# Kernel tuning notes

Measured on AMD Instinct MI355X. Metric: run time of the kernel, lower is better.

The kernel has to match this reference:

```python
import jax, jax.numpy as jnp
import numpy as np

H = 256; NH = 4; DH = H // NH
NT, NS, NV = 4096, 2048, 1024
E1, E2, E3 = 65536, 16384, 32768
LN_EPS = 1e-5


def setup_inputs() -> dict:
    key = jax.random.key(0)
    ks = jax.random.split(key, 40)
    def nrm(i, shape):
        return jax.random.normal(ks[i], shape, jnp.float32) * 0.05
    inp = {
        "x_term": jax.random.normal(ks[0], (NT, H), jnp.float32),
        "x_symbol": jax.random.normal(ks[1], (NS, H), jnp.float32),
        "x_var": jax.random.normal(ks[2], (NV, H), jnp.float32),
        "ha_src": jax.random.randint(ks[3], (E1,), 0, NT),
        "ha_dst": jax.random.randint(ks[4], (E1,), 0, NT),
        "so_src": jax.random.randint(ks[5], (E2,), 0, NT),
        "so_dst": jax.random.randint(ks[6], (E2,), 0, NS),
        "vo_src": jax.random.randint(ks[7], (E3,), 0, NV),
        "vo_dst": jax.random.randint(ks[8], (E3,), 0, NT),
        # SAGEConv params for the 4 term-destination relations
        "Wl_rha": nrm(9, (H, H)),  "bl_rha": nrm(10, (H,)), "Wr_rha": nrm(11, (H, H)),
        "Wl_ha":  nrm(12, (H, H)), "bl_ha":  nrm(13, (H,)), "Wr_ha":  nrm(14, (H, H)),
        "Wl_rsym": nrm(15, (H, H)), "bl_rsym": nrm(16, (H,)), "Wr_rsym": nrm(17, (H, H)),
        "Wl_var": nrm(18, (H, H)), "bl_var": nrm(19, (H,)), "Wr_var": nrm(20, (H, H)),
        "ln_g": jnp.ones((H,), jnp.float32),
        "ln_b": jnp.zeros((H,), jnp.float32),
        "in_proj_w": nrm(21, (3 * H, H)),
        "in_proj_b": nrm(22, (3 * H,)),
        "out_proj_w": nrm(23, (H, H)),
        "out_proj_b": nrm(24, (H,)),
        "post_w": nrm(25, (H, H)),
        "post_b": nrm(26, (H,)),
    }
    return inp


def _sage(x_src, x_dst, src, dst, Wl, bl, Wr, num_dst):
    # PyG SAGEConv: lin_l(mean_j x_src[j]) + lin_r(x_dst)
    msg = x_src[src]                                            # [E, H] gather
    s = jax.ops.segment_sum(msg, dst, num_segments=num_dst)     # [N_dst, H] scatter-add
    cnt = jax.ops.segment_sum(jnp.ones((src.shape[0],), x_src.dtype), dst,
                              num_segments=num_dst)
    agg = s / jnp.maximum(cnt, 1.0)[:, None]
    return agg @ Wl.T + bl + x_dst @ Wr.T


def _layernorm(x, g, b):
    mu = jnp.mean(x, axis=-1, keepdims=True)
    var = jnp.mean(jnp.square(x - mu), axis=-1, keepdims=True)
    return (x - mu) * jax.lax.rsqrt(var + LN_EPS) * g + b


def _mha(x, in_w, in_b, out_w, out_b):
    # torch MultiheadAttention (eval, batch=1, self-attention)
    qkv = x @ in_w.T + in_b                       # [N, 3H]
    q, k, v = jnp.split(qkv, 3, axis=-1)
    def heads(t):
        return t.reshape(-1, NH, DH).transpose(1, 0, 2)  # [NH, N, DH]
    q, k, v = heads(q), heads(k), heads(v)
    scores = jnp.einsum("hqd,hkd->hqk", q, k) / np.sqrt(DH).astype(np.float32)
    a = jax.nn.softmax(scores, axis=-1)
    o = jnp.einsum("hqk,hkd->hqd", a, v)          # [NH, N, DH]
    o = o.transpose(1, 0, 2).reshape(-1, H)
    return o @ out_w.T + out_b


def reference(x_term, x_symbol, x_var,
              ha_src, ha_dst, so_src, so_dst, vo_src, vo_dst,
              Wl_rha, bl_rha, Wr_rha, Wl_ha, bl_ha, Wr_ha,
              Wl_rsym, bl_rsym, Wr_rsym, Wl_var, bl_var, Wr_var,
              ln_g, ln_b, in_proj_w, in_proj_b, out_proj_w, out_proj_b,
              post_w, post_b):
    nt = x_term.shape[0]
    # HeteroConv(aggr='sum') over the 4 relations whose destination is 'term'
    conv_term = (
        _sage(x_term, x_term, ha_dst, ha_src, Wl_rha, bl_rha, Wr_rha, nt)    # rev_has_arg
        + _sage(x_term, x_term, ha_src, ha_dst, Wl_ha, bl_ha, Wr_ha, nt)     # has_arg
        + _sage(x_symbol, x_term, so_dst, so_src, Wl_rsym, bl_rsym, Wr_rsym, nt)  # rev_symbol_of
        + _sage(x_var, x_term, vo_src, vo_dst, Wl_var, bl_var, Wr_var, nt)   # var_occurrence
    )
    term_out = _layernorm(conv_term + x_term, ln_g, ln_b)  # dropout is identity in eval
    attn_out = _mha(term_out, in_proj_w, in_proj_b, out_proj_w, out_proj_b)
    post = jax.nn.relu(attn_out @ post_w.T + post_b)
    term_final = post + term_out
    return term_final
```

## Files before the change

kernel.cpp:

```cpp
#include <hip/hip_runtime.h>
#include <hip/hip_bf16.h>

#define H 256
#define NT 4096
#define NHEAD 4
#define E1 65536
#define E2 16384
#define E3 32768
#define TOTE (2 * E1 + E2 + E3)
#define LN_EPS 1e-5f
#define SPLIT 4

typedef __hip_bfloat16 bf16;
typedef short bf16x8 __attribute__((ext_vector_type(8)));
typedef float f32x4 __attribute__((ext_vector_type(4)));

__device__ __forceinline__ float b2f(bf16 v) { return __bfloat162float(v); }
__device__ __forceinline__ float u2f(unsigned short u) {
    unsigned int x = ((unsigned int)u) << 16;
    return __uint_as_float(x);
}
__device__ __forceinline__ unsigned short f2u(float f) {
    bf16 h = __float2bfloat16(f);
    unsigned short v;
    __builtin_memcpy(&v, &h, 2);
    return v;
}
__device__ __forceinline__ float ldin(const void* p, size_t i, bool isbf) {
    return isbf ? b2f(((const bf16*)p)[i]) : ((const float*)p)[i];
}
__device__ __forceinline__ void gload_lds16(const void* g, void* l) {
    __builtin_amdgcn_global_load_lds(
        (const __attribute__((address_space(1))) unsigned int*)g,
        (__attribute__((address_space(3))) unsigned int*)l, 16, 0, 0);
}

__global__ __launch_bounds__(256) void k_count4(const int* __restrict__ s0, const int* __restrict__ s1,
                                                const int* __restrict__ s2, const int* __restrict__ s3,
                                                int* __restrict__ cnt) {
    int i = blockIdx.x * 256 + threadIdx.x;
    int r, e;
    if (i < E1) { r = 0; e = i; }
    else if (i < 2 * E1) { r = 1; e = i - E1; }
    else if (i < 2 * E1 + E2) { r = 2; e = i - 2 * E1; }
    else if (i < TOTE) { r = 3; e = i - 2 * E1 - E2; }
    else return;
    const int* s = (r == 0) ? s0 : (r == 1) ? s1 : (r == 2) ? s2 : s3;
    atomicAdd(&cnt[r * NT + s[e]], 1);
}

__global__ __launch_bounds__(256) void k_scan(const int* __restrict__ cnt, int* __restrict__ offs,
                                              int* __restrict__ cursor,
                                              const unsigned int* __restrict__ lng,
                                              unsigned int* __restrict__ flag) {
    __shared__ int tot[256];
    int t = threadIdx.x, r = blockIdx.x;
    if (r == 0 && t == 0) *flag = (lng[0] == 0x3F803F80u) ? 1u : 0u;
    const int* c = cnt + r * NT;
    int* o = offs + r * (NT + 1);
    int* cur = cursor + r * NT;
    int base = t * 16;
    int local[16];
    int sum = 0;
#pragma unroll
    for (int j = 0; j < 16; j++) { local[j] = c[base + j]; sum += local[j]; }
    tot[t] = sum;
    __syncthreads();
    if (t == 0) {
        int run = 0;
        for (int i = 0; i < 256; i++) { int v = tot[i]; tot[i] = run; run += v; }
        o[NT] = run;
    }
    __syncthreads();
    int run = tot[t];
#pragma unroll
    for (int j = 0; j < 16; j++) { o[base + j] = run; cur[base + j] = run; run += local[j]; }
}

__global__ __launch_bounds__(256) void k_fill(const int* __restrict__ s0, const int* __restrict__ s1,
                                              const int* __restrict__ s2, const int* __restrict__ s3,
                                              const int* __restrict__ g0, const int* __restrict__ g1,
                                              const int* __restrict__ g2, const int* __restrict__ g3,
                                              int* __restrict__ cursor, int* __restrict__ csr) {
    int i = blockIdx.x * 256 + threadIdx.x;
    int r, e, rb;
    if (i < E1) { r = 0; e = i; rb = 0; }
    else if (i < 2 * E1) { r = 1; e = i - E1; rb = E1; }
    else if (i < 2 * E1 + E2) { r = 2; e = i - 2 * E1; rb = 2 * E1; }
    else if (i < TOTE) { r = 3; e = i - 2 * E1 - E2; rb = 2 * E1 + E2; }
    else return;
    const int* s = (r == 0) ? s0 : (r == 1) ? s1 : (r == 2) ? s2 : s3;
    const int* g = (r == 0) ? g0 : (r == 1) ? g1 : (r == 2) ? g2 : g3;
    int d = s[e];
    int pos = atomicAdd(&cursor[r * NT + d], 1);
    csr[rb + pos] = g[e];
}

__global__ __launch_bounds__(256) void k_gprep(
    const void* __restrict__ x0, const void* __restrict__ x1,
    const void* __restrict__ x2, const void* __restrict__ x3,
    const int* __restrict__ offs, const int* __restrict__ csr,
    bf16* __restrict__ aggs,
    const void* __restrict__ Wl0, const void* __restrict__ Wl1,
    const void* __restrict__ Wl2, const void* __restrict__ Wl3,
    const void* __restrict__ Wr0, const void* __restrict__ Wr1,
    const void* __restrict__ Wr2, const void* __restrict__ Wr3,
    const void* __restrict__ bb0, const void* __restrict__ bb1,
    const void* __restrict__ bb2, const void* __restrict__ bb3,
    bf16* __restrict__ Bcat, float* __restrict__ bsum,
    const unsigned int* __restrict__ flag) {
    const int bid = blockIdx.x, tid = threadIdx.x;
    const bool isbf = (*flag != 0u);
    if (bid < 4096) {
        int y = bid >> 10;
        int i = (bid & 1023) * 4 + (tid >> 6);
        int lane = tid & 63;
        const void* x = (y == 0) ? x0 : (y == 1) ? x1 : (y == 2) ? x2 : x3;
        static const int rbase[4] = {0, E1, 2 * E1, 2 * E1 + E2};
        const int* o = offs + y * (NT + 1);
        const int* cs = csr + rbase[y];
        int b = o[i], e = o[i + 1];
        float ax = 0.f, ay = 0.f, az = 0.f, aw = 0.f;
        float bx = 0.f, by = 0.f, bz = 0.f, bw = 0.f;
        int j = b;
        if (isbf) {
            for (; j + 2 <= e; j += 2) {
                int s0 = cs[j], s1 = cs[j + 1];
                ushort4 u0 = *(const ushort4*)((const unsigned short*)x + (size_t)s0 * H + lane * 4);
                ushort4 u1 = *(const ushort4*)((const unsigned short*)x + (size_t)s1 * H + lane * 4);
                ax += u2f(u0.x); ay += u2f(u0.y); az += u2f(u0.z); aw += u2f(u0.w);
                bx += u2f(u1.x); by += u2f(u1.y); bz += u2f(u1.z); bw += u2f(u1.w);
            }
            if (j < e) {
                int s = cs[j];
                ushort4 u = *(const ushort4*)((const unsigned short*)x + (size_t)s * H + lane * 4);
                ax += u2f(u.x); ay += u2f(u.y); az += u2f(u.z); aw += u2f(u.w);
            }
        } else {
            for (; j + 2 <= e; j += 2) {
                int s0 = cs[j], s1 = cs[j + 1];
                float4 v0 = *(const float4*)((const float*)x + (size_t)s0 * H + lane * 4);
                float4 v1 = *(const float4*)((const float*)x + (size_t)s1 * H + lane * 4);
                ax += v0.x; ay += v0.y; az += v0.z; aw += v0.w;
                bx += v1.x; by += v1.y; bz += v1.z; bw += v1.w;
            }
            if (j < e) {
                int s = cs[j];
                float4 v = *(const float4*)((const float*)x + (size_t)s * H + lane * 4);
                ax += v.x; ay += v.y; az += v.z; aw += v.w;
            }
        }
        ax += bx; ay += by; az += bz; aw += bw;
        float inv = 1.0f / fmaxf((float)(e - b), 1.0f);
        *(ushort4*)((unsigned short*)aggs + ((size_t)y * NT + i) * H + lane * 4) =
            make_ushort4(f2u(ax * inv), f2u(ay * inv), f2u(az * inv), f2u(aw * inv));
    } else {
        int idx = (bid - 4096) * 256 + tid;
        int n = idx / 1280, k = idx % 1280;
        float v;
        if (k < 1024) {
            const void* W = (k < 256) ? Wl0 : (k < 512) ? Wl1 : (k < 768) ? Wl2 : Wl3;
            v = ldin(W, (size_t)n * 256 + (k & 255), isbf);
        } else {
            size_t o = (size_t)n * 256 + (k - 1024);
            v = ldin(Wr0, o, isbf) + ldin(Wr1, o, isbf) + ldin(Wr2, o, isbf) + ldin(Wr3, o, isbf);
        }
        ((unsigned short*)Bcat)[idx] = f2u(v);
        if (idx < 256)
            bsum[idx] = ldin(bb0, idx, isbf) + ldin(bb1, idx, isbf) +
                        ldin(bb2, idx, isbf) + ldin(bb3, idx, isbf);
    }
}

__global__ __launch_bounds__(256) void k_convln(
    const bf16* __restrict__ aggs, const bf16* __restrict__ Bcat, const float* __restrict__ bsum,
    const void* __restrict__ xt, const void* __restrict__ gw, const void* __restrict__ gb,
    bf16* __restrict__ term, const unsigned int* __restrict__ flag) {
    __shared__ unsigned short Asm[160 * 16 * 8];
    __shared__ unsigned short Bsm[2][8 * 256 * 8];
    __shared__ float redS[4][16];
    const bool isbf = (*flag != 0u);
    const int tid = threadIdx.x;
    const int w = tid >> 6, lane = tid & 63;
    const int col = lane & 15, quad = lane >> 4;
    const int m0 = blockIdx.x * 16;

#pragma unroll
    for (int t = 0; t < 8; t++) {
        int c2 = t * 256 + tid;
        int row = c2 & 15, kq = c2 >> 4;
        gload_lds16((const unsigned short*)aggs + ((size_t)(kq >> 5) * NT + m0 + row) * 256 + (kq & 31) * 8,
                    &Asm[(t * 256 + w * 64) * 8]);
    }
    if (isbf) {
#pragma unroll
        for (int t = 8; t < 10; t++) {
            int c2 = t * 256 + tid;
            int row = c2 & 15, kq = c2 >> 4;
            gload_lds16((const unsigned short*)xt + (size_t)(m0 + row) * 256 + (kq - 128) * 8,
                        &Asm[(t * 256 + w * 64) * 8]);
        }
    } else {
#pragma unroll
        for (int t = 8; t < 10; t++) {
            int c2 = t * 256 + tid;
            int row = c2 & 15, kq = c2 >> 4;
            const float* xf = (const float*)xt;
            bf16x8 a;
#pragma unroll
            for (int j = 0; j < 8; j++)
                a[j] = (short)f2u(xf[(size_t)(m0 + row) * 256 + (kq - 128) * 8 + j]);
            *(bf16x8*)&Asm[c2 * 8] = a;
        }
    }
    asm volatile("s_waitcnt vmcnt(0) lgkmcnt(0)" ::: "memory");
    __builtin_amdgcn_s_barrier();

    auto stageB = [&](int k0, int buf) {
#pragma unroll
        for (int t = 0; t < 8; t++) {
            gload_lds16((const unsigned short*)Bcat + (size_t)tid * 1280 + k0 + t * 8,
                        &Bsm[buf][(t * 256 + w * 64) * 8]);
        }
    };
    f32x4 acc[4];
#pragma unroll
    for (int dt = 0; dt < 4; dt++) acc[dt] = (f32x4){0.f, 0.f, 0.f, 0.f};

    stageB(0, 0);
    stageB(64, 1);
    for (int k0 = 0; k0 < 1280; k0 += 64) {
        const int cur = (k0 >> 6) & 1;
        if (k0 + 64 < 1280) {
            asm volatile("s_waitcnt vmcnt(8)" ::: "memory");
        } else {
            asm volatile("s_waitcnt vmcnt(0)" ::: "memory");
        }
        __builtin_amdgcn_s_barrier();
        __builtin_amdgcn_sched_barrier(0);
#pragma unroll
        for (int ch = 0; ch < 2; ch++) {
            bf16x8 a = *(const bf16x8*)&Asm[(((k0 >> 3) + ch * 4 + quad) * 16 + col) * 8];
#pragma unroll
            for (int dt = 0; dt < 4; dt++) {
                bf16x8 b = *(const bf16x8*)&Bsm[cur][((ch * 4 + quad) * 256 + w * 64 + dt * 16 + col) * 8];
                acc[dt] = __builtin_amdgcn_mfma_f32_16x16x32_bf16(a, b, acc[dt], 0, 0, 0);
            }
        }
        __builtin_amdgcn_sched_barrier(0);
        __builtin_amdgcn_s_barrier();
        if (k0 + 128 < 1280) stageB(k0 + 128, cur);
    }

#pragma unroll
    for (int dt = 0; dt < 4; dt++) {
        int n = w * 64 + dt * 16 + col;
        float bsv = bsum[n];
#pragma unroll
        for (int r = 0; r < 4; r++) {
            int m = m0 + quad * 4 + r;
            acc[dt][r] += bsv + ldin(xt, (size_t)m * 256 + n, isbf);
        }
    }
    float mu[4], rs_[4];
#pragma unroll
    for (int r = 0; r < 4; r++) {
        float s = acc[0][r] + acc[1][r] + acc[2][r] + acc[3][r];
#pragma unroll
        for (int mk = 1; mk <= 8; mk <<= 1) s += __shfl_xor(s, mk);
        if (col == 0) redS[w][quad * 4 + r] = s;
    }
    __syncthreads();
#pragma unroll
    for (int r = 0; r < 4; r++) {
        int m = quad * 4 + r;
        mu[r] = (redS[0][m] + redS[1][m] + redS[2][m] + redS[3][m]) * (1.0f / 256.0f);
    }
    __syncthreads();
#pragma unroll
    for (int r = 0; r < 4; r++) {
        float s2 = 0.f;
#pragma unroll
        for (int dt = 0; dt < 4; dt++) {
            float d = acc[dt][r] - mu[r];
            s2 += d * d;
        }
#pragma unroll
        for (int mk = 1; mk <= 8; mk <<= 1) s2 += __shfl_xor(s2, mk);
        if (col == 0) redS[w][quad * 4 + r] = s2;
    }
    __syncthreads();
#pragma unroll
    for (int r = 0; r < 4; r++) {
        int m = quad * 4 + r;
        float var = (redS[0][m] + redS[1][m] + redS[2][m] + redS[3][m]) * (1.0f / 256.0f);
        rs_[r] = rsqrtf(var + LN_EPS);
    }
#pragma unroll
    for (int dt = 0; dt < 4; dt++) {
        int n = w * 64 + dt * 16 + col;
        float gv = ldin(gw, n, isbf), bv = ldin(gb, n, isbf);
#pragma unroll
        for (int r = 0; r < 4; r++) {
            int m = m0 + quad * 4 + r;
            term[(size_t)m * 256 + n] = __float2bfloat16((acc[dt][r] - mu[r]) * rs_[r] * gv + bv);
        }
    }
}

template <int AMODE, int EPI>
__global__ __launch_bounds__(256) void k_gemm(
    const void* __restrict__ A, const void* __restrict__ A2, const float* __restrict__ ml,
    const void* __restrict__ B, const void* __restrict__ bias,
    const bf16* __restrict__ resid, bf16* __restrict__ vt, void* __restrict__ outp,
    int M, int N, int K, const unsigned int* __restrict__ flag) {
    __shared__ unsigned short Asm[32 * 64 * 8];
    __shared__ unsigned short Bsm[32 * 64 * 8];
    const bool isbf = (*flag != 0u);
    const int tid = threadIdx.x;
    const int w = tid >> 6, lane = tid & 63;
    const int col = lane & 15, quad = lane >> 4;
    const int m0 = blockIdx.x * 64, n0 = blockIdx.y * 64;
    const int srow = tid & 63, skq = tid >> 6;
    const int am = m0 + srow;

    if (AMODE == 0) {
#pragma unroll
        for (int c = 0; c < 8; c++) {
            gload_lds16((const unsigned short*)A + (size_t)(m0 + lane) * K + skq * 64 + c * 8,
                        &Asm[((skq * 8 + c) * 64) * 8]);
        }
    } else {
        float l0 = ml[(size_t)(0 * NHEAD + skq) * NT + am];
        float l1 = ml[(size_t)(1 * NHEAD + skq) * NT + am];
        float l2 = ml[(size_t)(2 * NHEAD + skq) * NT + am];
        float l3 = ml[(size_t)(3 * NHEAD + skq) * NT + am];
        float iw = 1.0f / (l0 + l1 + l2 + l3);
#pragma unroll
        for (int c = 0; c < 8; c++) {
            int k = skq * 64 + c * 8;
            bf16x8 o0 = *(const bf16x8*)((const unsigned short*)A + (size_t)am * H + k);
            bf16x8 o1 = *(const bf16x8*)((const unsigned short*)A + ((size_t)NT + am) * H + k);
            bf16x8 o2 = *(const bf16x8*)((const unsigned short*)A2 + (size_t)am * H + k);
            bf16x8 o3 = *(const bf16x8*)((const unsigned short*)A2 + ((size_t)NT + am) * H + k);
            bf16x8 areg;
#pragma unroll
            for (int j = 0; j < 8; j++)
                areg[j] = (short)f2u((l0 * u2f((unsigned short)o0[j]) + l1 * u2f((unsigned short)o1[j]) +
                                      l2 * u2f((unsigned short)o2[j]) + l3 * u2f((unsigned short)o3[j])) * iw);
            *(bf16x8*)&Asm[((skq * 8 + c) * 64 + srow) * 8] = areg;
        }
    }
    if (isbf) {
#pragma unroll
        for (int c = 0; c < 8; c++) {
            gload_lds16((const unsigned short*)B + (size_t)(n0 + lane) * K + skq * 64 + c * 8,
                        &Bsm[((skq * 8 + c) * 64) * 8]);
        }
    } else {
#pragma unroll
        for (int c = 0; c < 8; c++) {
            size_t bi = (size_t)(n0 + srow) * K + skq * 64 + c * 8;
            bf16x8 breg;
#pragma unroll
            for (int j = 0; j < 8; j++) breg[j] = (short)f2u(((const float*)B)[bi + j]);
            *(bf16x8*)&Bsm[((skq * 8 + c) * 64 + srow) * 8] = breg;
        }
    }
    __syncthreads();

    f32x4 acc[4];
#pragma unroll
    for (int dt = 0; dt < 4; dt++) acc[dt] = (f32x4){0.f, 0.f, 0.f, 0.f};
#pragma unroll
    for (int kk = 0; kk < 8; kk++) {
        bf16x8 a = *(const bf16x8*)&Asm[((kk * 4 + quad) * 64 + w * 16 + col) * 8];
#pragma unroll
        for (int dt = 0; dt < 4; dt++) {
            bf16x8 b = *(const bf16x8*)&Bsm[((kk * 4 + quad) * 64 + dt * 16 + col) * 8];
            acc[dt] = __builtin_amdgcn_mfma_f32_16x16x32_bf16(a, b, acc[dt], 0, 0, 0);
        }
    }
#pragma unroll
    for (int dt = 0; dt < 4; dt++) {
        int n = n0 + dt * 16 + col;
        float bv = ldin(bias, n, isbf);
        if (EPI == 3 && n0 >= 512) {
            int m = m0 + w * 16 + quad * 4;
            *(ushort4*)((unsigned short*)vt + (size_t)(n - 512) * NT + m) =
                make_ushort4(f2u(acc[dt][0] + bv), f2u(acc[dt][1] + bv),
                             f2u(acc[dt][2] + bv), f2u(acc[dt][3] + bv));
            continue;
        }
#pragma unroll
        for (int r = 0; r < 4; r++) {
            int m = m0 + w * 16 + quad * 4 + r;
            float v = acc[dt][r] + bv;
            if (EPI == 3) {
                ((bf16*)outp)[(size_t)m * 512 + n] = __float2bfloat16(v);
            } else if (EPI == 2) {
                size_t off = (size_t)m * N + n;
                v = fmaxf(v, 0.f);
                v += b2f(resid[off]);
                ((float*)outp)[off] = v;
            } else {
                ((bf16*)outp)[(size_t)m * N + n] = __float2bfloat16(v);
            }
        }
    }
    (void)M;
}

__global__ __launch_bounds__(256) void k_attn(const bf16* __restrict__ qkvQK,
                                              const bf16* __restrict__ vt,
                                              bf16* __restrict__ opart01,
                                              bf16* __restrict__ opart23,
                                              float* __restrict__ ml) {
    __shared__ unsigned short Ksm[2][8 * 64 * 8];
    __shared__ unsigned short Vsm[2][8 * 64 * 8];
    const int h = blockIdx.y, sp = blockIdx.z;
    const int q0 = blockIdx.x * 64;
    const int tid = threadIdx.x;
    const int w = tid >> 6, lane = tid & 63;
    const int col = lane & 15, quad = lane >> 4;
    const unsigned short* qk = (const unsigned short*)qkvQK;
    const unsigned short* vp = (const unsigned short*)vt;

    bf16x8 aQ[2];
#pragma unroll
    for (int ch = 0; ch < 2; ch++)
        aQ[ch] = *(const bf16x8*)(qk + (size_t)(q0 + w * 16 + col) * 512 +
                                  h * 64 + ch * 32 + quad * 8);

    f32x4 O[4];
#pragma unroll
    for (int dt = 0; dt < 4; dt++) O[dt] = (f32x4){0.f, 0.f, 0.f, 0.f};
    float lsum = 0.f;

    const int kbeg = sp * (NT / SPLIT), kend = kbeg + NT / SPLIT;
    const float SC = 0.125f * 1.44269504f;

    auto stage = [&](int kb, int buf) {
#pragma unroll
        for (int it = 0; it < 2; it++) {
            int dhq = it * 4 + w;
            gload_lds16(qk + (size_t)(kb + lane) * 512 + 256 + h * 64 + dhq * 8,
                        &Ksm[buf][(it * 256 + w * 64) * 8]);
            gload_lds16(vp + (size_t)(h * 64 + lane) * NT + kb + dhq * 8,
                        &Vsm[buf][(it * 256 + w * 64) * 8]);
        }
    };

    stage(kbeg, 0);
    stage(kbeg + 64, 1);
    for (int kb = kbeg; kb < kend; kb += 64) {
        const int cur = ((kb - kbeg) >> 6) & 1;
        if (kb + 64 < kend) {
            asm volatile("s_waitcnt vmcnt(4)" ::: "memory");
        } else {
            asm volatile("s_waitcnt vmcnt(0)" ::: "memory");
        }
        __builtin_amdgcn_s_barrier();
        __builtin_amdgcn_sched_barrier(0);

        f32x4 c[4];
        __builtin_amdgcn_s_setprio(1);
#pragma unroll
        for (int dt = 0; dt < 4; dt++) {
            c[dt] = (f32x4){0.f, 0.f, 0.f, 0.f};
#pragma unroll
            for (int ch = 0; ch < 2; ch++) {
                bf16x8 kf = *(const bf16x8*)&Ksm[cur][((ch * 4 + quad) * 64 + dt * 16 + col) * 8];
                c[dt] = __builtin_amdgcn_mfma_f32_16x16x32_bf16(kf, aQ[ch], c[dt], 0, 0, 0);
            }
        }
        __builtin_amdgcn_s_setprio(0);

        float pp[4][4];
#pragma unroll
        for (int dt = 0; dt < 4; dt++) {
#pragma unroll
            for (int r = 0; r < 4; r++) {
                pp[dt][r] = __builtin_amdgcn_exp2f(c[dt][r] * SC);
            }
            lsum += (pp[dt][0] + pp[dt][1]) + (pp[dt][2] + pp[dt][3]);
        }

        union PU { unsigned int u[4]; bf16x8 v; };
        PU ap[2];
#pragma unroll
        for (int kc = 0; kc < 2; kc++) {
            unsigned int a0, a1, b0, b1;
            asm("v_cvt_pk_bf16_f32 %0, %1, %2" : "=v"(a0) : "v"(pp[2 * kc][0]), "v"(pp[2 * kc][1]));
            asm("v_cvt_pk_bf16_f32 %0, %1, %2" : "=v"(a1) : "v"(pp[2 * kc][2]), "v"(pp[2 * kc][3]));
            asm("v_cvt_pk_bf16_f32 %0, %1, %2" : "=v"(b0) : "v"(pp[2 * kc + 1][0]), "v"(pp[2 * kc + 1][1]));
            asm("v_cvt_pk_bf16_f32 %0, %1, %2" : "=v"(b1) : "v"(pp[2 * kc + 1][2]), "v"(pp[2 * kc + 1][3]));
            asm("v_permlane32_swap_b32 %0, %1" : "+v"(a0), "+v"(b0));
            asm("v_permlane16_swap_b32 %0, %1" : "+v"(a0), "+v"(b0));
            asm("v_permlane32_swap_b32 %0, %1" : "+v"(a1), "+v"(b1));
            asm("v_permlane16_swap_b32 %0, %1" : "+v"(a1), "+v"(b1));
            ap[kc].u[0] = a0; ap[kc].u[1] = a1; ap[kc].u[2] = b0; ap[kc].u[3] = b1;
        }

        __builtin_amdgcn_s_setprio(1);
#pragma unroll
        for (int dt = 0; dt < 4; dt++)
#pragma unroll
            for (int kc = 0; kc < 2; kc++) {
                bf16x8 b = *(const bf16x8*)&Vsm[cur][((kc * 4 + quad) * 64 + dt * 16 + col) * 8];
                O[dt] = __builtin_amdgcn_mfma_f32_16x16x32_bf16(ap[kc].v, b, O[dt], 0, 0, 0);
            }
        __builtin_amdgcn_s_setprio(0);

        __builtin_amdgcn_sched_barrier(0);
        __builtin_amdgcn_s_barrier();
        if (kb + 128 < kend) stage(kb + 128, cur);
    }
    float l = lsum;
    l += __shfl_xor(l, 16);
    l += __shfl_xor(l, 32);
    bf16* ob = (sp < 2) ? (opart01 + (size_t)sp * NT * H) : (opart23 + (size_t)(sp - 2) * NT * H);
    if (quad == 0)
        ml[((size_t)sp * NHEAD + h) * NT + (q0 + w * 16 + col)] = l;
    float lr[4];
#pragma unroll
    for (int r = 0; r < 4; r++) lr[r] = __shfl(l, quad * 4 + r, 16);
#pragma unroll
    for (int dt = 0; dt < 4; dt++) {
#pragma unroll
        for (int r = 0; r < 4; r++) {
            int q = q0 + w * 16 + quad * 4 + r;
            ob[(size_t)q * H + h * 64 + dt * 16 + col] = __float2bfloat16(O[dt][r] / lr[r]);
        }
    }
}

extern "C" void kernel_launch(void* const* d_in, const int* in_sizes, int n_in,
                              void* d_out, int out_size, void* d_ws, size_t ws_size,
                              hipStream_t stream) {
    const void* x_term   = d_in[0];
    const void* x_symbol = d_in[1];
    const void* x_var    = d_in[2];
    const int* ha_src = (const int*)d_in[3];
    const int* ha_dst = (const int*)d_in[4];
    const int* so_src = (const int*)d_in[5];
    const int* so_dst = (const int*)d_in[6];
    const int* vo_src = (const int*)d_in[7];
    const int* vo_dst = (const int*)d_in[8];
    const void* Wl[4]  = {d_in[9],  d_in[12], d_in[15], d_in[18]};
    const void* blv[4] = {d_in[10], d_in[13], d_in[16], d_in[19]};
    const void* Wr[4]  = {d_in[11], d_in[14], d_in[17], d_in[20]};
    const void* ln_g = d_in[21];
    const void* ln_b = d_in[22];
    const void* in_w = d_in[23];
    const void* in_b = d_in[24];
    const void* out_w = d_in[25];
    const void* out_b = d_in[26];
    const void* post_w = d_in[27];
    const void* post_b = d_in[28];

    char* ws = (char*)d_ws;
    unsigned int* flag = (unsigned int*)ws;
    char* csrbase = ws + 256;
    int* cnt    = (int*)csrbase;
    int* offs   = (int*)(csrbase + 65536);
    int* cursor = (int*)(csrbase + 132096);
    int* csr    = (int*)(csrbase + 197632);
    bf16*  Bcat = (bf16*)csrbase;
    float* bsum = (float*)(csrbase + 655360);
    float* ml   = (float*)csrbase;
    bf16* aggs  = (bf16*)(ws + (1 << 20));
    bf16* term  = (bf16*)(ws + (1 << 20) + 8388608);
    bf16* opart23 = (bf16*)(ws + (1 << 20) + 10485760);
    bf16* qkvQK = aggs;
    bf16* vt    = (bf16*)((char*)aggs + 4194304);
    bf16* proj  = aggs;
    bf16* opart01 = (bf16*)d_out;

    hipMemsetAsync(cnt, 0, 4 * NT * sizeof(int), stream);
    k_count4<<<(TOTE + 255) / 256, 256, 0, stream>>>(ha_src, ha_dst, so_src, vo_dst, cnt);
    k_scan<<<4, 256, 0, stream>>>(cnt, offs, cursor, (const unsigned int*)ln_g, flag);
    k_fill<<<(TOTE + 255) / 256, 256, 0, stream>>>(ha_src, ha_dst, so_src, vo_dst,
                                                   ha_dst, ha_src, so_dst, vo_src, cursor, csr);

    k_gprep<<<4096 + 1280, 256, 0, stream>>>(
        x_term, x_term, x_symbol, x_var, offs, csr, aggs,
        Wl[0], Wl[1], Wl[2], Wl[3], Wr[0], Wr[1], Wr[2], Wr[3],
        blv[0], blv[1], blv[2], blv[3], Bcat, bsum, flag);

    k_convln<<<256, 256, 0, stream>>>(aggs, Bcat, bsum, x_term, ln_g, ln_b, term, flag);

    k_gemm<0, 3><<<dim3(64, 12), 256, 0, stream>>>(
        term, nullptr, nullptr, in_w, in_b, nullptr, vt, qkvQK, NT, 768, 256, flag);

    k_attn<<<dim3(64, NHEAD, SPLIT), 256, 0, stream>>>(qkvQK, vt, opart01, opart23, ml);

    k_gemm<1, 0><<<dim3(64, 4), 256, 0, stream>>>(
        opart01, opart23, ml, out_w, out_b, nullptr, nullptr, proj, NT, 256, 256, flag);

    k_gemm<0, 2><<<dim3(64, 4), 256, 0, stream>>>(
        proj, nullptr, nullptr, post_w, post_b, term, nullptr, d_out, NT, 256, 256, flag);

    (void)in_sizes; (void)n_in; (void)out_size; (void)ws_size;
}
```

Before: 273.6 us.

## Split fused conv+LayerNorm into 64x64-tiled GEMM and separate LN kernel

The fused kernel used 16-row tiles covering all 256 output columns, so every block re-streamed the full 1280x256 weight matrix. It is replaced by a 64x64-tiled GEMM over 256 blocks that writes fp32 results to a scratch buffer, followed by a row-wise LayerNorm kernel that adds bias and residual. This cuts redundant weight traffic and register/LDS pressure, at the cost of an extra launch, an fp32 round trip through memory, and losing the double-buffered B pipeline (staging is now synchronous).

Result: faster. 257.6 us (median of 2 runs) (-5.8%).

```diff
diff --git a/kernel.cpp b/kernel.cpp
--- a/kernel.cpp
+++ b/kernel.cpp
@@ -172,140 +172,104 @@
     }
 }
 
-__global__ __launch_bounds__(256) void k_convln(
-    const bf16* __restrict__ aggs, const bf16* __restrict__ Bcat, const float* __restrict__ bsum,
-    const void* __restrict__ xt, const void* __restrict__ gw, const void* __restrict__ gb,
-    bf16* __restrict__ term, const unsigned int* __restrict__ flag) {
-    __shared__ unsigned short Asm[160 * 16 * 8];
-    __shared__ unsigned short Bsm[2][8 * 256 * 8];
-    __shared__ float redS[4][16];
+__global__ __launch_bounds__(256) void k_conv(
+    const bf16* __restrict__ aggs, const void* __restrict__ xt,
+    const bf16* __restrict__ Bcat, float* __restrict__ convf32,
+    const unsigned int* __restrict__ flag) {
+    __shared__ unsigned short Asm[32 * 64 * 8];
+    __shared__ unsigned short Bsm[32 * 64 * 8];
     const bool isbf = (*flag != 0u);
     const int tid = threadIdx.x;
     const int w = tid >> 6, lane = tid & 63;
     const int col = lane & 15, quad = lane >> 4;
-    const int m0 = blockIdx.x * 16;
-
-#pragma unroll
-    for (int t = 0; t < 8; t++) {
-        int c2 = t * 256 + tid;
-        int row = c2 & 15, kq = c2 >> 4;
-        gload_lds16((const unsigned short*)aggs + ((size_t)(kq >> 5) * NT + m0 + row) * 256 + (kq & 31) * 8,
-                    &Asm[(t * 256 + w * 64) * 8]);
-    }
-    if (isbf) {
-#pragma unroll
-        for (int t = 8; t < 10; t++) {
-            int c2 = t * 256 + tid;
-            int row = c2 & 15, kq = c2 >> 4;
-            gload_lds16((const unsigned short*)xt + (size_t)(m0 + row) * 256 + (kq - 128) * 8,
-                        &Asm[(t * 256 + w * 64) * 8]);
-        }
-    } else {
-#pragma unroll
-        for (int t = 8; t < 10; t++) {
-            int c2 = t * 256 + tid;
-            int row = c2 & 15, kq = c2 >> 4;
-            const float* xf = (const float*)xt;
-            bf16x8 a;
-#pragma unroll
-            for (int j = 0; j < 8; j++)
-                a[j] = (short)f2u(xf[(size_t)(m0 + row) * 256 + (kq - 128) * 8 + j]);
-            *(bf16x8*)&Asm[c2 * 8] = a;
-        }
-    }
-    asm volatile("s_waitcnt vmcnt(0) lgkmcnt(0)" ::: "memory");
-    __builtin_amdgcn_s_barrier();
-
-    auto stageB = [&](int k0, int buf) {
-#pragma unroll
-        for (int t = 0; t < 8; t++) {
-            gload_lds16((const unsigned short*)Bcat + (size_t)tid * 1280 + k0 + t * 8,
-                        &Bsm[buf][(t * 256 + w * 64) * 8]);
-        }
-    };
+    const int m0 = blockIdx.x * 64, n0 = blockIdx.y * 64;
+    const int srow = tid & 63, skq = tid >> 6;
+
     f32x4 acc[4];
 #pragma unroll
     for (int dt = 0; dt < 4; dt++) acc[dt] = (f32x4){0.f, 0.f, 0.f, 0.f};
 
-    stageB(0, 0);
-    stageB(64, 1);
-    for (int k0 = 0; k0 < 1280; k0 += 64) {
-        const int cur = (k0 >> 6) & 1;
-        if (k0 + 64 < 1280) {
-            asm volatile("s_waitcnt vmcnt(8)" ::: "memory");
+    for (int p = 0; p < 5; p++) {
+        if (p < 4) {
+#pragma unroll
+            for (int c = 0; c < 8; c++)
+                gload_lds16((const unsigned short*)aggs + ((size_t)p * NT + m0 + lane) * 256 + skq * 64 + c * 8,
+                            &Asm[((skq * 8 + c) * 64) * 8]);
+        } else if (isbf) {
+#pragma unroll
+            for (int c = 0; c < 8; c++)
+                gload_lds16((const unsigned short*)xt + (size_t)(m0 + lane) * 256 + skq * 64 + c * 8,
+                            &Asm[((skq * 8 + c) * 64) * 8]);
         } else {
-            asm volatile("s_waitcnt vmcnt(0)" ::: "memory");
-        }
-        __builtin_amdgcn_s_barrier();
-        __builtin_amdgcn_sched_barrier(0);
-#pragma unroll
-        for (int ch = 0; ch < 2; ch++) {
-            bf16x8 a = *(const bf16x8*)&Asm[(((k0 >> 3) + ch * 4 + quad) * 16 + col) * 8];
+#pragma unroll
+            for (int c = 0; c < 8; c++) {
+                const float* xf = (const float*)xt;
+                bf16x8 a;
+#pragma unroll
+                for (int j = 0; j < 8; j++)
+                    a[j] = (short)f2u(xf[(size_t)(m0 + srow) * 256 + skq * 64 + c * 8 + j]);
+                *(bf16x8*)&Asm[((skq * 8 + c) * 64 + srow) * 8] = a;
+            }
+        }
+#pragma unroll
+        for (int c = 0; c < 8; c++)
+            gload_lds16((const unsigned short*)Bcat + (size_t)(n0 + lane) * 1280 + p * 256 + skq * 64 + c * 8,
+                        &Bsm[((skq * 8 + c) * 64) * 8]);
+        __syncthreads();
+
+#pragma unroll
+        for (int kk = 0; kk < 8; kk++) {
+            bf16x8 a = *(const bf16x8*)&Asm[((kk * 4 + quad) * 64 + w * 16 + col) * 8];
 #pragma unroll
             for (int dt = 0; dt < 4; dt++) {
-                bf16x8 b = *(const bf16x8*)&Bsm[cur][((ch * 4 + quad) * 256 + w * 64 + dt * 16 + col) * 8];
+                bf16x8 b = *(const bf16x8*)&Bsm[((kk * 4 + quad) * 64 + dt * 16 + col) * 8];
                 acc[dt] = __builtin_amdgcn_mfma_f32_16x16x32_bf16(a, b, acc[dt], 0, 0, 0);
             }
         }
-        __builtin_amdgcn_sched_barrier(0);
-        __builtin_amdgcn_s_barrier();
-        if (k0 + 128 < 1280) stageB(k0 + 128, cur);
-    }
-
+        if (p + 1 < 5) __syncthreads();
+    }
 #pragma unroll
     for (int dt = 0; dt < 4; dt++) {
-        int n = w * 64 + dt * 16 + col;
-        float bsv = bsum[n];
+        int n = n0 + dt * 16 + col;
 #pragma unroll
         for (int r = 0; r < 4; r++) {
-            int m = m0 + quad * 4 + r;
-            acc[dt][r] += bsv + ldin(xt, (size_t)m * 256 + n, isbf);
-        }
-    }
-    float mu[4], rs_[4];
-#pragma unroll
-    for (int r = 0; r < 4; r++) {
-        float s = acc[0][r] + acc[1][r] + acc[2][r] + acc[3][r];
-#pragma unroll
-        for (int mk = 1; mk <= 8; mk <<= 1) s += __shfl_xor(s, mk);
-        if (col == 0) redS[w][quad * 4 + r] = s;
-    }
-    __syncthreads();
-#pragma unroll
-    for (int r = 0; r < 4; r++) {
-        int m = quad * 4 + r;
-        mu[r] = (redS[0][m] + redS[1][m] + redS[2][m] + redS[3][m]) * (1.0f / 256.0f);
-    }
-    __syncthreads();
-#pragma unroll
-    for (int r = 0; r < 4; r++) {
-        float s2 = 0.f;
-#pragma unroll
-        for (int dt = 0; dt < 4; dt++) {
-            float d = acc[dt][r] - mu[r];
-            s2 += d * d;
-        }
-#pragma unroll
-        for (int mk = 1; mk <= 8; mk <<= 1) s2 += __shfl_xor(s2, mk);
-        if (col == 0) redS[w][quad * 4 + r] = s2;
-    }
-    __syncthreads();
-#pragma unroll
-    for (int r = 0; r < 4; r++) {
-        int m = quad * 4 + r;
-        float var = (redS[0][m] + redS[1][m] + redS[2][m] + redS[3][m]) * (1.0f / 256.0f);
-        rs_[r] = rsqrtf(var + LN_EPS);
-    }
-#pragma unroll
-    for (int dt = 0; dt < 4; dt++) {
-        int n = w * 64 + dt * 16 + col;
-        float gv = ldin(gw, n, isbf), bv = ldin(gb, n, isbf);
-#pragma unroll
-        for (int r = 0; r < 4; r++) {
-            int m = m0 + quad * 4 + r;
-            term[(size_t)m * 256 + n] = __float2bfloat16((acc[dt][r] - mu[r]) * rs_[r] * gv + bv);
-        }
-    }
+            int m = m0 + w * 16 + quad * 4 + r;
+            convf32[(size_t)m * 256 + n] = acc[dt][r];
+        }
+    }
+}
+
+__global__ __launch_bounds__(256) void k_ln(
+    const float* __restrict__ conv, const float* __restrict__ bsum,
+    const void* __restrict__ xt, const void* __restrict__ gw, const void* __restrict__ gb,
+    bf16* __restrict__ term, const unsigned int* __restrict__ flag) {
+    const int w = threadIdx.x >> 6, lane = threadIdx.x & 63;
+    const int m = blockIdx.x * 4 + w;
+    const bool isbf = (*flag != 0u);
+    const int n0 = lane * 4;
+    float4 cv = *(const float4*)(conv + (size_t)m * 256 + n0);
+    float4 bs = *(const float4*)(bsum + n0);
+    float v[4];
+#pragma unroll
+    for (int j = 0; j < 4; j++)
+        v[j] = ((&cv.x)[j]) + ((&bs.x)[j]) + ldin(xt, (size_t)m * 256 + n0 + j, isbf);
+    float s = (v[0] + v[1]) + (v[2] + v[3]);
+#pragma unroll
+    for (int mk = 1; mk <= 32; mk <<= 1) s += __shfl_xor(s, mk);
+    float mu = s * (1.0f / 256.0f);
+    float s2 = 0.f;
+#pragma unroll
+    for (int j = 0; j < 4; j++) { float d = v[j] - mu; s2 += d * d; }
+#pragma unroll
+    for (int mk = 1; mk <= 32; mk <<= 1) s2 += __shfl_xor(s2, mk);
+    float rs = rsqrtf(s2 * (1.0f / 256.0f) + LN_EPS);
+    unsigned short o[4];
+#pragma unroll
+    for (int j = 0; j < 4; j++) {
+        float gv = ldin(gw, n0 + j, isbf), bv = ldin(gb, n0 + j, isbf);
+        o[j] = f2u((v[j] - mu) * rs * gv + bv);
+    }
+    *(ushort4*)((unsigned short*)term + (size_t)m * 256 + n0) = make_ushort4(o[0], o[1], o[2], o[3]);
 }
 
 template <int AMODE, int EPI>
@@ -572,6 +536,7 @@
     bf16* aggs  = (bf16*)(ws + (1 << 20));
     bf16* term  = (bf16*)(ws + (1 << 20) + 8388608);
     bf16* opart23 = (bf16*)(ws + (1 << 20) + 10485760);
+    float* convf32 = (float*)opart23;
     bf16* qkvQK = aggs;
     bf16* vt    = (bf16*)((char*)aggs + 4194304);
     bf16* proj  = aggs;
@@ -588,7 +553,8 @@
         Wl[0], Wl[1], Wl[2], Wl[3], Wr[0], Wr[1], Wr[2], Wr[3],
         blv[0], blv[1], blv[2], blv[3], Bcat, bsum, flag);
 
-    k_convln<<<256, 256, 0, stream>>>(aggs, Bcat, bsum, x_term, ln_g, ln_b, term, flag);
+    k_conv<<<dim3(64, 4), 256, 0, stream>>>(aggs, x_term, Bcat, convf32, flag);
+    k_ln<<<1024, 256, 0, stream>>>(convf32, bsum, x_term, ln_g, ln_b, term, flag);
 
     k_gemm<0, 3><<<dim3(64, 12), 256, 0, stream>>>(
         term, nullptr, nullptr, in_w, in_b, nullptr, vt, qkvQK, NT, 768, 256, flag);
```
